# Kernel tuning notes

Hardware: AMD Instinct MI355X
Metric: run time of the kernel (lower is better)

Reference implementation:

```python
import jax, jax.numpy as jnp
import numpy as np

L, D, H, V, S, HID = 4, 1024, 16, 32000, 2048, 2816
HD = D // H  # 64
EPS = 1e-5


def setup_inputs() -> dict:
    key = jax.random.key(0)
    ks = jax.random.split(key, 10)
    s = 0.02  # init scale for numerical sanity; math is unaffected
    return {
        "tokens": jax.random.randint(ks[0], (1, S), 0, V),
        "emb": jax.random.normal(ks[1], (V, D), jnp.float32) * s,
        "wq": jax.random.normal(ks[2], (L, D, D), jnp.float32) * s,
        "wk": jax.random.normal(ks[3], (L, D, D), jnp.float32) * s,
        "wv": jax.random.normal(ks[4], (L, D, D), jnp.float32) * s,
        "wo": jax.random.normal(ks[5], (L, D, D), jnp.float32) * s,
        "w1": jax.random.normal(ks[6], (L, HID, D), jnp.float32) * s,
        "w2": jax.random.normal(ks[7], (L, D, HID), jnp.float32) * s,
        "w3": jax.random.normal(ks[8], (L, HID, D), jnp.float32) * s,
        "attn_norm_w": jnp.ones((L, D), jnp.float32),
        "ffn_norm_w": jnp.ones((L, D), jnp.float32),
        "final_norm_w": jnp.ones((D,), jnp.float32),
    }


def _rmsnorm(x, w):
    return x * jax.lax.rsqrt(jnp.mean(x * x, axis=-1, keepdims=True) + EPS) * w


def _rope(x, cos, sin):
    # x: [B,S,H,HD]; interleaved pairs (..., -1, 2) as in apply_rotary_emb
    xr, xi = x[..., 0::2], x[..., 1::2]
    outr = xr * cos - xi * sin
    outi = xr * sin + xi * cos
    return jnp.stack([outr, outi], axis=-1).reshape(x.shape)


def reference(tokens, emb, wq, wk, wv, wo, w1, w2, w3, attn_norm_w, ffn_norm_w, final_norm_w):
    # precompute_freqs_cis(head_dim, seq)
    inv_freq = 1.0 / (10000.0 ** (jnp.arange(0, HD, 2, dtype=jnp.float32) / HD))
    fr = jnp.outer(jnp.arange(S, dtype=jnp.float32), inv_freq)  # [S, HD/2]
    cos = jnp.cos(fr)[None, :, None, :]
    sin = jnp.sin(fr)[None, :, None, :]
    mask = jnp.triu(jnp.full((S, S), -jnp.inf, jnp.float32), k=1)
    scale = 1.0 / jnp.sqrt(jnp.float32(HD))

    h = emb[tokens]  # [B,S,D] embedding lookup (dropout p=0 -> identity)
    B = h.shape[0]

    def block(h, p):
        Wq, Wk, Wv, Wo, W1, W2, W3, anw, fnw = p
        x = _rmsnorm(h, anw)
        q = (x @ Wq.T).reshape(B, S, H, HD)
        k = (x @ Wk.T).reshape(B, S, H, HD)
        v = (x @ Wv.T).reshape(B, S, H, HD)
        q = _rope(q, cos, sin)
        k = _rope(k, cos, sin)
        q, k, v = (t.transpose(0, 2, 1, 3) for t in (q, k, v))  # [B,H,S,HD]
        scores = jnp.einsum("bhqd,bhkd->bhqk", q, k) * scale + mask
        attn = jax.nn.softmax(scores, axis=-1)
        o = jnp.einsum("bhqk,bhkd->bhqd", attn, v)
        o = o.transpose(0, 2, 1, 3).reshape(B, S, D)
        h = h + o @ Wo.T
        y = _rmsnorm(h, fnw)
        ff = (jax.nn.silu(y @ W1.T) * (y @ W3.T)) @ W2.T
        return h + ff, None

    h, _ = jax.lax.scan(block, h, (wq, wk, wv, wo, w1, w2, w3, attn_norm_w, ffn_norm_w))
    h = _rmsnorm(h, final_norm_w)
    logits = h[:, -1:, :] @ emb.T  # output weight tied to tok_embeddings; last position only
    return logits
```

## Files before the change

kernel.cpp:

```cpp
#include <hip/hip_runtime.h>

#define LNUM 4
#define DIM 1024
#define NH 16
#define VOCAB 32000
#define SEQ 2048
#define HIDD 2816

typedef _Float16 f16;
typedef _Float16 h8_t __attribute__((ext_vector_type(8)));
typedef _Float16 h4_t __attribute__((ext_vector_type(4)));
typedef float f4_t __attribute__((ext_vector_type(4)));

#define MFMA(a, b, c) __builtin_amdgcn_mfma_f32_16x16x32_f16(a, b, c, 0, 0, 0)

__device__ __forceinline__ void async16(void* lds, const void* g) {
  __builtin_amdgcn_global_load_lds(
      (const __attribute__((address_space(1))) void*)g,
      (__attribute__((address_space(3))) void*)lds, 16, 0, 0);
}

template <int N>
__device__ __forceinline__ float ror16(float x) {
  int r = __builtin_amdgcn_update_dpp(0, __builtin_bit_cast(int, x),
                                      0x120 | N, 0xF, 0xF, true);
  return __builtin_bit_cast(float, r);
}
__device__ __forceinline__ float rmax16(float v) {
  v = fmaxf(v, ror16<1>(v));
  v = fmaxf(v, ror16<2>(v));
  v = fmaxf(v, ror16<4>(v));
  v = fmaxf(v, ror16<8>(v));
  return v;
}
__device__ __forceinline__ float rsum16(float v) {
  v += ror16<1>(v);
  v += ror16<2>(v);
  v += ror16<4>(v);
  v += ror16<8>(v);
  return v;
}

__global__ __launch_bounds__(256) void cast_layer_k(
    const float* __restrict__ wq, const float* __restrict__ wk,
    const float* __restrict__ wv, const float* __restrict__ wo,
    const float* __restrict__ w1, const float* __restrict__ w3,
    const float* __restrict__ w2, f16* __restrict__ wqkv,
    f16* __restrict__ wod, f16* __restrict__ w13, f16* __restrict__ w2d) {
  const int DD4c = DIM * DIM / 4, HD4c = HIDD * DIM / 4;
  int i = blockIdx.x * 256 + threadIdx.x;
  const float* s;
  f16* d;
  int si, di;
  if (i < 3 * DD4c) {
    d = wqkv;
    di = i;
    if (i < DD4c) {
      s = wq; si = i;
    } else if (i < 2 * DD4c) {
      s = wk; si = i - DD4c;
    } else {
      s = wv; si = i - 2 * DD4c;
    }
  } else if (i < 4 * DD4c) {
    s = wo; si = i - 3 * DD4c; d = wod; di = si;
  } else if (i < 4 * DD4c + HD4c) {
    s = w1; si = i - 4 * DD4c; d = w13; di = si;
  } else if (i < 4 * DD4c + 2 * HD4c) {
    s = w3; si = i - 4 * DD4c - HD4c; d = w13; di = si + HD4c;
  } else {
    s = w2; si = i - 4 * DD4c - 2 * HD4c; d = w2d; di = si;
  }
  float4 v = ((const float4*)s)[si];
  ((h4_t*)d)[di] = (h4_t){(f16)v.x, (f16)v.y, (f16)v.z, (f16)v.w};
}

__global__ __launch_bounds__(256) void embed_k(const int* __restrict__ tok,
                                               const float* __restrict__ emb,
                                               float* __restrict__ h) {
  const int s = blockIdx.x, t = threadIdx.x;
  ((float4*)(h + (size_t)s * DIM))[t] =
      ((const float4*)(emb + (size_t)tok[s] * DIM))[t];
}

__global__ void rope_tab_k(float* __restrict__ tab) {
  int i = blockIdx.x * 256 + threadIdx.x;
  if (i >= SEQ * 32) return;
  int s = i >> 5, f = i & 31;
  float inv = powf(10000.f, -(float)f * (1.f / 32.f));
  float a = (float)s * inv;
  float sn, c;
  sincosf(a, &sn, &c);
  tab[i * 2] = c;
  tab[i * 2 + 1] = sn;
}

__global__ __launch_bounds__(256) void rope_k(f16* __restrict__ qkv,
                                              const float* __restrict__ tab) {
  int i = blockIdx.x * 256 + threadIdx.x;
  int f = i & 31, hh = (i >> 5) & 15, part = (i >> 9) & 1, s = i >> 10;
  size_t base = (size_t)s * 3072 + part * 1024 + hh * 64 + f * 2;
  float xr = (float)qkv[base], xi = (float)qkv[base + 1];
  float c = tab[(s * 32 + f) * 2], sn = tab[(s * 32 + f) * 2 + 1];
  qkv[base] = (f16)(xr * c - xi * sn);
  qkv[base + 1] = (f16)(xr * sn + xi * c);
}

__global__ __launch_bounds__(256) void rmsnorm_k(const float* __restrict__ h,
                                                 const float* __restrict__ w,
                                                 f16* __restrict__ out) {
  const int s = blockIdx.x, t = threadIdx.x;
  float4 v = ((const float4*)(h + (size_t)s * DIM))[t];
  float ss = v.x * v.x + v.y * v.y + v.z * v.z + v.w * v.w;
#pragma unroll
  for (int d = 1; d < 64; d <<= 1) ss += __shfl_xor(ss, d);
  __shared__ float red[4];
  if ((t & 63) == 0) red[t >> 6] = ss;
  __syncthreads();
  float tot = red[0] + red[1] + red[2] + red[3];
  float sc = rsqrtf(tot * (1.f / (float)DIM) + 1e-5f);
  float4 wv = ((const float4*)w)[t];
  ((h4_t*)(out + (size_t)s * DIM))[t] =
      (h4_t){(f16)(v.x * sc * wv.x), (f16)(v.y * sc * wv.y),
             (f16)(v.z * sc * wv.z), (f16)(v.w * sc * wv.w)};
}

__global__ __launch_bounds__(256) void final_norm_k(const float* __restrict__ h,
                                                    const float* __restrict__ w,
                                                    float* __restrict__ hn) {
  const int t = threadIdx.x;
  float4 v = ((const float4*)(h + (size_t)(SEQ - 1) * DIM))[t];
  float ss = v.x * v.x + v.y * v.y + v.z * v.z + v.w * v.w;
#pragma unroll
  for (int d = 1; d < 64; d <<= 1) ss += __shfl_xor(ss, d);
  __shared__ float red[4];
  if ((t & 63) == 0) red[t >> 6] = ss;
  __syncthreads();
  float tot = red[0] + red[1] + red[2] + red[3];
  float sc = rsqrtf(tot * (1.f / (float)DIM) + 1e-5f);
  float4 wv = ((const float4*)w)[t];
  ((float4*)hn)[t] = make_float4(v.x * sc * wv.x, v.y * sc * wv.y,
                                 v.z * sc * wv.z, v.w * sc * wv.w);
}

__global__ __launch_bounds__(256) void logits_k(const float* __restrict__ hn,
                                                const float* __restrict__ emb,
                                                float* __restrict__ out) {
  const int v = blockIdx.x * 4 + (threadIdx.x >> 6);
  const int lane = threadIdx.x & 63;
  const float4* er = (const float4*)(emb + (size_t)v * DIM);
  const float4* hr = (const float4*)hn;
  float s = 0.f;
#pragma unroll
  for (int i = 0; i < 4; i++) {
    float4 a = er[lane + i * 64];
    float4 b = hr[lane + i * 64];
    s += a.x * b.x + a.y * b.y + a.z * b.z + a.w * b.w;
  }
#pragma unroll
  for (int d = 1; d < 64; d <<= 1) s += __shfl_xor(s, d);
  if (lane == 0) out[v] = s;
}

__global__ __launch_bounds__(256) void silu_k(const f16* __restrict__ g13,
                                              f16* __restrict__ t) {
  int c = blockIdx.x * 256 + threadIdx.x;
  int s = blockIdx.y;
  float g = (float)g13[(size_t)s * (2 * HIDD) + c];
  float u = (float)g13[(size_t)s * (2 * HIDD) + HIDD + c];
  float r = g / (1.f + __expf(-g)) * u;
  t[(size_t)s * HIDD + c] = (f16)r;
}

__global__ __launch_bounds__(256) void transpose_v(const f16* __restrict__ qkv,
                                                   f16* __restrict__ vT) {
  __shared__ f16 tile[32][34];
  int bs = blockIdx.x * 32;
  int bc = blockIdx.y * 32;
  int tx = threadIdx.x & 31, ty = threadIdx.x >> 5;
#pragma unroll
  for (int i = ty; i < 32; i += 8)
    tile[i][tx] = qkv[(size_t)(bs + i) * 3072 + 2048 + bc + tx];
  __syncthreads();
#pragma unroll
  for (int i = ty; i < 32; i += 8)
    vT[(size_t)(bc + i) * SEQ + bs + tx] = tile[tx][i];
}

template <int EPI>
__global__ __launch_bounds__(256) void gemm_bt(const f16* __restrict__ A,
                                               const f16* __restrict__ B,
                                               void* __restrict__ Cout, int M,
                                               int N, int K) {
  __shared__ __align__(16) f16 As[128 * 32];
  __shared__ __align__(16) f16 Bs[128 * 32];
  const int t = threadIdx.x;
  const int lane = t & 63;
  const int wave = t >> 6;
  const int wr = wave >> 1, wc = wave & 1;
  const int bm = blockIdx.x, bn = blockIdx.y;
  const int lr = lane & 15, lk = lane >> 4;

  const int srow = t >> 2;
  const int scol = (t & 3) * 8;
  const f16* gA = A + (size_t)(bm * 128 + srow) * K + scol;
  const f16* gB = B + (size_t)(bn * 128 + srow) * K + scol;
  f16* lA = As + t * 8;
  f16* lB = Bs + t * 8;

  f4_t acc[4][4];
#pragma unroll
  for (int m = 0; m < 4; m++)
#pragma unroll
    for (int n = 0; n < 4; n++) acc[m][n] = {0.f, 0.f, 0.f, 0.f};

  for (int k0 = 0; k0 < K; k0 += 32) {
    __syncthreads();
    async16(lA, gA + k0);
    async16(lA + 64 * 32, gA + (size_t)64 * K + k0);
    async16(lB, gB + k0);
    async16(lB + 64 * 32, gB + (size_t)64 * K + k0);
    __syncthreads();
    h8_t af[4], bfr[4];
#pragma unroll
    for (int m = 0; m < 4; m++)
      af[m] = *(const h8_t*)(As + (wr * 64 + m * 16 + lr) * 32 + lk * 8);
#pragma unroll
    for (int n = 0; n < 4; n++)
      bfr[n] = *(const h8_t*)(Bs + (wc * 64 + n * 16 + lr) * 32 + lk * 8);
#pragma unroll
    for (int m = 0; m < 4; m++)
#pragma unroll
      for (int n = 0; n < 4; n++) acc[m][n] = MFMA(af[m], bfr[n], acc[m][n]);
  }

  const int orow = bm * 128 + wr * 64 + lk * 4;
  const int ocol = bn * 128 + wc * 64 + lr;
#pragma unroll
  for (int m = 0; m < 4; m++)
#pragma unroll
    for (int n = 0; n < 4; n++)
#pragma unroll
      for (int j = 0; j < 4; j++) {
        int r = orow + m * 16 + j;
        int c = ocol + n * 16;
        if (EPI == 0) {
          ((f16*)Cout)[(size_t)r * N + c] = (f16)acc[m][n][j];
        } else {
          float* pC = (float*)Cout + (size_t)r * N + c;
          *pC += acc[m][n][j];
        }
      }
}

__global__ __launch_bounds__(256) void gemm_skp(const f16* __restrict__ A,
                                                const f16* __restrict__ B,
                                                float* __restrict__ Cp, int N,
                                                int ld, int Ks) {
  __shared__ __align__(16) f16 As[128 * 32];
  __shared__ __align__(16) f16 Bs[128 * 32];
  const int t = threadIdx.x;
  const int lane = t & 63;
  const int wave = t >> 6;
  const int wr = wave >> 1, wc = wave & 1;
  const int bm = blockIdx.x, bn = blockIdx.y, bk = blockIdx.z;
  const int lr = lane & 15, lk = lane >> 4;

  const f16* Ao = A + (size_t)bk * Ks;
  const f16* Bo = B + (size_t)bk * Ks;
  float* Cout = Cp + (size_t)bk * gridDim.x * 128 * N;

  const int srow = t >> 2;
  const int scol = (t & 3) * 8;
  const f16* gA = Ao + (size_t)(bm * 128 + srow) * ld + scol;
  const f16* gB = Bo + (size_t)(bn * 128 + srow) * ld + scol;
  f16* lA = As + t * 8;
  f16* lB = Bs + t * 8;

  f4_t acc[4][4];
#pragma unroll
  for (int m = 0; m < 4; m++)
#pragma unroll
    for (int n = 0; n < 4; n++) acc[m][n] = {0.f, 0.f, 0.f, 0.f};

  for (int k0 = 0; k0 < Ks; k0 += 32) {
    __syncthreads();
    async16(lA, gA + k0);
    async16(lA + 64 * 32, gA + (size_t)64 * ld + k0);
    async16(lB, gB + k0);
    async16(lB + 64 * 32, gB + (size_t)64 * ld + k0);
    __syncthreads();
    h8_t af[4], bfr[4];
#pragma unroll
    for (int m = 0; m < 4; m++)
      af[m] = *(const h8_t*)(As + (wr * 64 + m * 16 + lr) * 32 + lk * 8);
#pragma unroll
    for (int n = 0; n < 4; n++)
      bfr[n] = *(const h8_t*)(Bs + (wc * 64 + n * 16 + lr) * 32 + lk * 8);
#pragma unroll
    for (int m = 0; m < 4; m++)
#pragma unroll
      for (int n = 0; n < 4; n++) acc[m][n] = MFMA(af[m], bfr[n], acc[m][n]);
  }

  const int orow = bm * 128 + wr * 64 + lk * 4;
  const int ocol = bn * 128 + wc * 64 + lr;
#pragma unroll
  for (int m = 0; m < 4; m++)
#pragma unroll
    for (int n = 0; n < 4; n++)
#pragma unroll
      for (int j = 0; j < 4; j++)
        Cout[(size_t)(orow + m * 16 + j) * N + ocol + n * 16] = acc[m][n][j];
}

__global__ __launch_bounds__(256) void sk_reduce_k(const float* __restrict__ p,
                                                   float* __restrict__ h,
                                                   int n4) {
  int i = blockIdx.x * 256 + threadIdx.x;
  if (i >= n4) return;
  float4 a = ((const float4*)p)[i];
  float4 b = ((const float4*)p)[i + n4];
  float4 c = ((float4*)h)[i];
  c.x += a.x + b.x;
  c.y += a.y + b.y;
  c.z += a.z + b.z;
  c.w += a.w + b.w;
  ((float4*)h)[i] = c;
}

__global__ __launch_bounds__(256) void attn_k(const f16* __restrict__ qkv,
                                              const f16* __restrict__ vT,
                                              f16* __restrict__ o) {
  const int hh = blockIdx.x;
  const int qb = blockIdx.y;
  const int tid = threadIdx.x;
  const int wave = tid >> 6;
  const int lane = tid & 63;
  const int lr = lane & 15, lk = lane >> 4;
  const int q0 = qb * 32;
  __shared__ __align__(16) char P[4][4096];
  __shared__ float MB[3][64][48];

  h8_t qf[2][2];
#pragma unroll
  for (int m = 0; m < 2; m++)
#pragma unroll
    for (int ks = 0; ks < 2; ks++)
      qf[m][ks] = *(const h8_t*)(qkv + (size_t)(q0 + m * 16 + lr) * 3072 +
                                 hh * 64 + ks * 32 + lk * 8);

  float mrow[2][4], lsum[2][4];
  f4_t oacc[2][4];
#pragma unroll
  for (int m = 0; m < 2; m++)
#pragma unroll
    for (int j = 0; j < 4; j++) {
      mrow[m][j] = -1e30f;
      lsum[m][j] = 0.f;
    }
#pragma unroll
  for (int m = 0; m < 2; m++)
#pragma unroll
    for (int n = 0; n < 4; n++) oacc[m][n] = {0.f, 0.f, 0.f, 0.f};

  const int ntiles = (qb >> 1) + 1;
  char* Pw = P[wave];
  for (int kt = wave; kt < ntiles; kt += 4) {
    f4_t sacc[2][4];
#pragma unroll
    for (int m = 0; m < 2; m++)
#pragma unroll
      for (int n = 0; n < 4; n++) sacc[m][n] = {0.f, 0.f, 0.f, 0.f};
#pragma unroll
    for (int ks = 0; ks < 2; ks++) {
      h8_t kf[4];
#pragma unroll
      for (int n = 0; n < 4; n++)
        kf[n] = *(const h8_t*)(qkv + (size_t)(kt * 64 + n * 16 + lr) * 3072 +
                               1024 + hh * 64 + ks * 32 + lk * 8);
#pragma unroll
      for (int m = 0; m < 2; m++)
#pragma unroll
        for (int n = 0; n < 4; n++)
          sacc[m][n] = MFMA(qf[m][ks], kf[n], sacc[m][n]);
    }
    const bool lastt = (kt == ntiles - 1);
    float pv[2][4][4];
#pragma unroll
    for (int m = 0; m < 2; m++)
#pragma unroll
      for (int n = 0; n < 4; n++)
#pragma unroll
        for (int j = 0; j < 4; j++) {
          float sv = sacc[m][n][j] * 0.125f;
          if (lastt && (kt * 64 + n * 16 + lr) > (q0 + m * 16 + lk * 4 + j))
            sv = -1e30f;
          pv[m][n][j] = sv;
        }
#pragma unroll
    for (int m = 0; m < 2; m++)
#pragma unroll
      for (int j = 0; j < 4; j++) {
        float mx = fmaxf(fmaxf(pv[m][0][j], pv[m][1][j]),
                         fmaxf(pv[m][2][j], pv[m][3][j]));
        mx = rmax16(mx);
        float mnew = fmaxf(mrow[m][j], mx);
        float corr = __expf(mrow[m][j] - mnew);
        mrow[m][j] = mnew;
        float rs = 0.f;
#pragma unroll
        for (int n = 0; n < 4; n++) {
          float pe = __expf(pv[m][n][j] - mnew);
          pv[m][n][j] = pe;
          rs += pe;
        }
        rs = rsum16(rs);
        lsum[m][j] = lsum[m][j] * corr + rs;
#pragma unroll
        for (int n = 0; n < 4; n++) oacc[m][n][j] *= corr;
      }
#pragma unroll
    for (int m = 0; m < 2; m++)
#pragma unroll
      for (int n = 0; n < 4; n++)
#pragma unroll
        for (int j = 0; j < 4; j++) {
          int r = m * 16 + lk * 4 + j, c = n * 16 + lr;
          int off = (r * 128 + c * 2) ^ ((r & 7) << 4);
          *(f16*)(Pw + off) = (f16)pv[m][n][j];
        }
#pragma unroll
    for (int ks = 0; ks < 2; ks++) {
      h8_t pf[2], vf[4];
#pragma unroll
      for (int m = 0; m < 2; m++) {
        int r = m * 16 + lr;
        int off = (r * 128 + ks * 64 + lk * 16) ^ ((r & 7) << 4);
        pf[m] = *(const h8_t*)(Pw + off);
      }
#pragma unroll
      for (int n = 0; n < 4; n++)
        vf[n] = *(const h8_t*)(vT + (size_t)(hh * 64 + n * 16 + lr) * SEQ +
                               kt * 64 + ks * 32 + lk * 8);
#pragma unroll
      for (int m = 0; m < 2; m++)
#pragma unroll
        for (int n = 0; n < 4; n++)
          oacc[m][n] = MFMA(pf[m], vf[n], oacc[m][n]);
    }
  }

  if (wave > 0) {
    float* d = &MB[wave - 1][lane][0];
#pragma unroll
    for (int m = 0; m < 2; m++)
#pragma unroll
      for (int j = 0; j < 4; j++) {
        d[m * 4 + j] = mrow[m][j];
        d[8 + m * 4 + j] = lsum[m][j];
      }
#pragma unroll
    for (int m = 0; m < 2; m++)
#pragma unroll
      for (int n = 0; n < 4; n++)
#pragma unroll
        for (int j = 0; j < 4; j++)
          d[16 + m * 16 + n * 4 + j] = oacc[m][n][j];
  }
  __syncthreads();
  if (wave == 0) {
#pragma unroll
    for (int m = 0; m < 2; m++)
#pragma unroll
      for (int j = 0; j < 4; j++) {
        float M = mrow[m][j];
#pragma unroll
        for (int w = 0; w < 3; w++) M = fmaxf(M, MB[w][lane][m * 4 + j]);
        float sc0 = __expf(mrow[m][j] - M);
        float L = lsum[m][j] * sc0;
        float scw[3];
#pragma unroll
        for (int w = 0; w < 3; w++) {
          scw[w] = __expf(MB[w][lane][m * 4 + j] - M);
          L += MB[w][lane][8 + m * 4 + j] * scw[w];
        }
        float invL = 1.f / L;
#pragma unroll
        for (int n = 0; n < 4; n++) {
          float val = oacc[m][n][j] * sc0;
#pragma unroll
          for (int w = 0; w < 3; w++)
            val += MB[w][lane][16 + m * 16 + n * 4 + j] * scw[w];
          o[(size_t)(q0 + m * 16 + lk * 4 + j) * DIM + hh * 64 + n * 16 + lr] =
              (f16)(val * invL);
        }
      }
  }
}

extern "C" void kernel_launch(void* const* d_in, const int* in_sizes, int n_in,
                              void* d_out, int out_size, void* d_ws,
                              size_t ws_size, hipStream_t stream) {
  (void)in_sizes; (void)n_in; (void)out_size; (void)ws_size;
  const int* tokens = (const int*)d_in[0];
  const float* emb = (const float*)d_in[1];
  const float* wq = (const float*)d_in[2];
  const float* wk = (const float*)d_in[3];
  const float* wv = (const float*)d_in[4];
  const float* wo = (const float*)d_in[5];
  const float* w1 = (const float*)d_in[6];
  const float* w2 = (const float*)d_in[7];
  const float* w3 = (const float*)d_in[8];
  const float* anw = (const float*)d_in[9];
  const float* fnw = (const float*)d_in[10];
  const float* finw = (const float*)d_in[11];
  float* out = (float*)d_out;

  char* p = (char*)d_ws;
  auto alloc = [&](size_t bytes) {
    char* r = p;
    p += (bytes + 255) & ~(size_t)255;
    return r;
  };
  f16* wqkv_l = (f16*)alloc((size_t)3 * DIM * DIM * 2);
  f16* wo_l = (f16*)alloc((size_t)DIM * DIM * 2);
  f16* w13_l = (f16*)alloc((size_t)2 * HIDD * DIM * 2);
  f16* w2_l = (f16*)alloc((size_t)DIM * HIDD * 2);
  float* hbuf = (float*)alloc((size_t)SEQ * DIM * 4);
  f16* x_h = (f16*)alloc((size_t)SEQ * DIM * 2);
  f16* qkv_h = (f16*)alloc((size_t)SEQ * 3 * DIM * 2);
  f16* vT_h = (f16*)alloc((size_t)DIM * SEQ * 2);
  f16* o_h = (f16*)alloc((size_t)SEQ * DIM * 2);
  f16* g13_h = (f16*)alloc((size_t)SEQ * 2 * HIDD * 2);
  f16* t_h = (f16*)alloc((size_t)SEQ * HIDD * 2);
  float* skbuf = (float*)alloc((size_t)2 * SEQ * DIM * 4);
  float* tab = (float*)alloc((size_t)SEQ * 32 * 2 * 4);
  float* hn = (float*)alloc(4096);

  embed_k<<<SEQ, 256, 0, stream>>>(tokens, emb, hbuf);
  rope_tab_k<<<(SEQ * 32 + 255) / 256, 256, 0, stream>>>(tab);

  const int CAST_BLOCKS = (4 * (DIM * DIM / 4) + 3 * (HIDD * DIM / 4)) / 256;
  const int N4 = SEQ * DIM / 4;
  for (int l = 0; l < LNUM; l++) {
    const size_t offDD = (size_t)l * DIM * DIM;
    const size_t offHD = (size_t)l * HIDD * DIM;
    cast_layer_k<<<CAST_BLOCKS, 256, 0, stream>>>(
        wq + offDD, wk + offDD, wv + offDD, wo + offDD, w1 + offHD,
        w3 + offHD, w2 + offHD, wqkv_l, wo_l, w13_l, w2_l);

    rmsnorm_k<<<SEQ, 256, 0, stream>>>(hbuf, anw + (size_t)l * DIM, x_h);
    {
      dim3 g(SEQ / 128, (3 * DIM) / 128);
      gemm_bt<0><<<g, 256, 0, stream>>>(x_h, wqkv_l, qkv_h, SEQ, 3 * DIM, DIM);
    }
    rope_k<<<(SEQ * 2 * NH * 32) / 256, 256, 0, stream>>>(qkv_h, tab);
    {
      dim3 g(SEQ / 32, DIM / 32);
      transpose_v<<<g, 256, 0, stream>>>(qkv_h, vT_h);
    }
    {
      dim3 g(NH, SEQ / 32);
      attn_k<<<g, 256, 0, stream>>>(qkv_h, vT_h, o_h);
    }
    {
      dim3 g(SEQ / 128, DIM / 128, 2);
      gemm_skp<<<g, 256, 0, stream>>>(o_h, wo_l, skbuf, DIM, DIM, DIM / 2);
      sk_reduce_k<<<(N4 + 255) / 256, 256, 0, stream>>>(skbuf, hbuf, N4);
    }
    rmsnorm_k<<<SEQ, 256, 0, stream>>>(hbuf, fnw + (size_t)l * DIM, x_h);
    {
      dim3 g(SEQ / 128, (2 * HIDD) / 128);
      gemm_bt<0><<<g, 256, 0, stream>>>(x_h, w13_l, g13_h, SEQ, 2 * HIDD, DIM);
    }
    {
      dim3 g(HIDD / 256, SEQ);
      silu_k<<<g, 256, 0, stream>>>(g13_h, t_h);
    }
    {
      dim3 g(SEQ / 128, DIM / 128, 2);
      gemm_skp<<<g, 256, 0, stream>>>(t_h, w2_l, skbuf, DIM, HIDD, HIDD / 2);
      sk_reduce_k<<<(N4 + 255) / 256, 256, 0, stream>>>(skbuf, hbuf, N4);
    }
  }
  final_norm_k<<<1, 256, 0, stream>>>(hbuf, finw, hn);
  logits_k<<<VOCAB / 4, 256, 0, stream>>>(hn, emb, out);
}
```

Measured before the change: 896.1 us.

## Fuse RoPE, SiLU-gate and split-K reduction into GEMM epilogues

Applies RoPE in the QKV GEMM epilogue via DPP lane swaps, and fuses the W1/W3 GEMMs with the SiLU gating into one kernel that holds two accumulator sets. The split-K GEMMs now atomically add straight into the residual buffer, so the partial-sum buffer and reduce kernel are gone. Attention merge scratch for O is stored in fp16 to cut LDS use. This removes several kernel launches and intermediate HBM round trips, at the cost of doubled accumulator registers in the W13 kernel, nondeterministic fp32 atomics, and slightly lower precision in the attention merge.

```diff
diff --git a/kernel.cpp b/kernel.cpp
--- a/kernel.cpp
+++ b/kernel.cpp
@@ -39,6 +39,11 @@
   v += ror16<4>(v);
   v += ror16<8>(v);
   return v;
+}
+__device__ __forceinline__ float qswap(float x) {
+  int r = __builtin_amdgcn_update_dpp(0, __builtin_bit_cast(int, x), 0xB1,
+                                      0xF, 0xF, true);
+  return __builtin_bit_cast(float, r);
 }
 
 __global__ __launch_bounds__(256) void cast_layer_k(
@@ -95,17 +100,6 @@
   tab[i * 2 + 1] = sn;
 }
 
-__global__ __launch_bounds__(256) void rope_k(f16* __restrict__ qkv,
-                                              const float* __restrict__ tab) {
-  int i = blockIdx.x * 256 + threadIdx.x;
-  int f = i & 31, hh = (i >> 5) & 15, part = (i >> 9) & 1, s = i >> 10;
-  size_t base = (size_t)s * 3072 + part * 1024 + hh * 64 + f * 2;
-  float xr = (float)qkv[base], xi = (float)qkv[base + 1];
-  float c = tab[(s * 32 + f) * 2], sn = tab[(s * 32 + f) * 2 + 1];
-  qkv[base] = (f16)(xr * c - xi * sn);
-  qkv[base + 1] = (f16)(xr * sn + xi * c);
-}
-
 __global__ __launch_bounds__(256) void rmsnorm_k(const float* __restrict__ h,
                                                  const float* __restrict__ w,
                                                  f16* __restrict__ out) {
@@ -162,16 +156,6 @@
   if (lane == 0) out[v] = s;
 }
 
-__global__ __launch_bounds__(256) void silu_k(const f16* __restrict__ g13,
-                                              f16* __restrict__ t) {
-  int c = blockIdx.x * 256 + threadIdx.x;
-  int s = blockIdx.y;
-  float g = (float)g13[(size_t)s * (2 * HIDD) + c];
-  float u = (float)g13[(size_t)s * (2 * HIDD) + HIDD + c];
-  float r = g / (1.f + __expf(-g)) * u;
-  t[(size_t)s * HIDD + c] = (f16)r;
-}
-
 __global__ __launch_bounds__(256) void transpose_v(const f16* __restrict__ qkv,
                                                    f16* __restrict__ vT) {
   __shared__ f16 tile[32][34];
@@ -187,11 +171,11 @@
     vT[(size_t)(bc + i) * SEQ + bs + tx] = tile[tx][i];
 }
 
-template <int EPI>
-__global__ __launch_bounds__(256) void gemm_bt(const f16* __restrict__ A,
-                                               const f16* __restrict__ B,
-                                               void* __restrict__ Cout, int M,
-                                               int N, int K) {
+__global__ __launch_bounds__(256) void gemm_qkv(const f16* __restrict__ A,
+                                                const f16* __restrict__ B,
+                                                f16* __restrict__ C,
+                                                const float* __restrict__ tab) {
+  const int N = 3 * DIM, K = DIM;
   __shared__ __align__(16) f16 As[128 * 32];
   __shared__ __align__(16) f16 Bs[128 * 32];
   const int t = threadIdx.x;
@@ -236,27 +220,102 @@
 
   const int orow = bm * 128 + wr * 64 + lk * 4;
   const int ocol = bn * 128 + wc * 64 + lr;
+  const float ssign = (lr & 1) ? 1.f : -1.f;
 #pragma unroll
   for (int m = 0; m < 4; m++)
 #pragma unroll
-    for (int n = 0; n < 4; n++)
+    for (int n = 0; n < 4; n++) {
+      const int c = ocol + n * 16;
+      const bool qk = c < 2048;
+      const int f = (n * 16 + lr) >> 1;
 #pragma unroll
       for (int j = 0; j < 4; j++) {
         int r = orow + m * 16 + j;
-        int c = ocol + n * 16;
-        if (EPI == 0) {
-          ((f16*)Cout)[(size_t)r * N + c] = (f16)acc[m][n][j];
-        } else {
-          float* pC = (float*)Cout + (size_t)r * N + c;
-          *pC += acc[m][n][j];
+        float sv = acc[m][n][j];
+        float pa = qswap(sv);
+        if (qk) {
+          float2 cs = ((const float2*)tab)[r * 32 + f];
+          sv = sv * cs.x + pa * cs.y * ssign;
         }
+        C[(size_t)r * N + c] = (f16)sv;
+      }
+    }
+}
+
+__global__ __launch_bounds__(256) void gemm_w13(const f16* __restrict__ A,
+                                                const f16* __restrict__ B13,
+                                                f16* __restrict__ T) {
+  const int K = DIM;
+  __shared__ __align__(16) f16 As[128 * 32];
+  __shared__ __align__(16) f16 B1s[128 * 32];
+  __shared__ __align__(16) f16 B3s[128 * 32];
+  const int t = threadIdx.x;
+  const int lane = t & 63;
+  const int wave = t >> 6;
+  const int wr = wave >> 1, wc = wave & 1;
+  const int bm = blockIdx.x, bn = blockIdx.y;
+  const int lr = lane & 15, lk = lane >> 4;
+
+  const int srow = t >> 2;
+  const int scol = (t & 3) * 8;
+  const f16* gA = A + (size_t)(bm * 128 + srow) * K + scol;
+  const f16* gB1 = B13 + (size_t)(bn * 128 + srow) * K + scol;
+  const f16* gB3 = B13 + (size_t)(HIDD + bn * 128 + srow) * K + scol;
+  f16* lA = As + t * 8;
+  f16* lB1 = B1s + t * 8;
+  f16* lB3 = B3s + t * 8;
+
+  f4_t acc1[4][4], acc3[4][4];
+#pragma unroll
+  for (int m = 0; m < 4; m++)
+#pragma unroll
+    for (int n = 0; n < 4; n++) {
+      acc1[m][n] = {0.f, 0.f, 0.f, 0.f};
+      acc3[m][n] = {0.f, 0.f, 0.f, 0.f};
+    }
+
+  for (int k0 = 0; k0 < K; k0 += 32) {
+    __syncthreads();
+    async16(lA, gA + k0);
+    async16(lA + 64 * 32, gA + (size_t)64 * K + k0);
+    async16(lB1, gB1 + k0);
+    async16(lB1 + 64 * 32, gB1 + (size_t)64 * K + k0);
+    async16(lB3, gB3 + k0);
+    async16(lB3 + 64 * 32, gB3 + (size_t)64 * K + k0);
+    __syncthreads();
+    h8_t af[4];
+#pragma unroll
+    for (int m = 0; m < 4; m++)
+      af[m] = *(const h8_t*)(As + (wr * 64 + m * 16 + lr) * 32 + lk * 8);
+#pragma unroll
+    for (int n = 0; n < 4; n++) {
+      h8_t b1 = *(const h8_t*)(B1s + (wc * 64 + n * 16 + lr) * 32 + lk * 8);
+#pragma unroll
+      for (int m = 0; m < 4; m++) acc1[m][n] = MFMA(af[m], b1, acc1[m][n]);
+      h8_t b3 = *(const h8_t*)(B3s + (wc * 64 + n * 16 + lr) * 32 + lk * 8);
+#pragma unroll
+      for (int m = 0; m < 4; m++) acc3[m][n] = MFMA(af[m], b3, acc3[m][n]);
+    }
+  }
+
+  const int orow = bm * 128 + wr * 64 + lk * 4;
+  const int ocol = bn * 128 + wc * 64 + lr;
+#pragma unroll
+  for (int m = 0; m < 4; m++)
+#pragma unroll
+    for (int n = 0; n < 4; n++)
+#pragma unroll
+      for (int j = 0; j < 4; j++) {
+        float g = acc1[m][n][j], u = acc3[m][n][j];
+        float r = g / (1.f + __expf(-g)) * u;
+        T[(size_t)(orow + m * 16 + j) * HIDD + ocol + n * 16] = (f16)r;
       }
 }
 
 __global__ __launch_bounds__(256) void gemm_skp(const f16* __restrict__ A,
                                                 const f16* __restrict__ B,
-                                                float* __restrict__ Cp, int N,
-                                                int ld, int Ks) {
+                                                float* __restrict__ H, int ld,
+                                                int Ks) {
   __shared__ __align__(16) f16 As[128 * 32];
   __shared__ __align__(16) f16 Bs[128 * 32];
   const int t = threadIdx.x;
@@ -268,7 +327,6 @@
 
   const f16* Ao = A + (size_t)bk * Ks;
   const f16* Bo = B + (size_t)bk * Ks;
-  float* Cout = Cp + (size_t)bk * gridDim.x * 128 * N;
 
   const int srow = t >> 2;
   const int scol = (t & 3) * 8;
@@ -311,22 +369,8 @@
     for (int n = 0; n < 4; n++)
 #pragma unroll
       for (int j = 0; j < 4; j++)
-        Cout[(size_t)(orow + m * 16 + j) * N + ocol + n * 16] = acc[m][n][j];
-}
-
-__global__ __launch_bounds__(256) void sk_reduce_k(const float* __restrict__ p,
-                                                   float* __restrict__ h,
-                                                   int n4) {
-  int i = blockIdx.x * 256 + threadIdx.x;
-  if (i >= n4) return;
-  float4 a = ((const float4*)p)[i];
-  float4 b = ((const float4*)p)[i + n4];
-  float4 c = ((float4*)h)[i];
-  c.x += a.x + b.x;
-  c.y += a.y + b.y;
-  c.z += a.z + b.z;
-  c.w += a.w + b.w;
-  ((float4*)h)[i] = c;
+        atomicAdd(H + (size_t)(orow + m * 16 + j) * DIM + ocol + n * 16,
+                  acc[m][n][j]);
 }
 
 __global__ __launch_bounds__(256) void attn_k(const f16* __restrict__ qkv,
@@ -340,7 +384,8 @@
   const int lr = lane & 15, lk = lane >> 4;
   const int q0 = qb * 32;
   __shared__ __align__(16) char P[4][4096];
-  __shared__ float MB[3][64][48];
+  __shared__ float MBml[3][64][16];
+  __shared__ f16 MBo[3][64][32];
 
   h8_t qf[2][2];
 #pragma unroll
@@ -452,13 +497,14 @@
   }
 
   if (wave > 0) {
-    float* d = &MB[wave - 1][lane][0];
+    float* dml = &MBml[wave - 1][lane][0];
+    f16* doo = &MBo[wave - 1][lane][0];
 #pragma unroll
     for (int m = 0; m < 2; m++)
 #pragma unroll
       for (int j = 0; j < 4; j++) {
-        d[m * 4 + j] = mrow[m][j];
-        d[8 + m * 4 + j] = lsum[m][j];
+        dml[m * 4 + j] = mrow[m][j];
+        dml[8 + m * 4 + j] = lsum[m][j];
       }
 #pragma unroll
     for (int m = 0; m < 2; m++)
@@ -466,7 +512,7 @@
       for (int n = 0; n < 4; n++)
 #pragma unroll
         for (int j = 0; j < 4; j++)
-          d[16 + m * 16 + n * 4 + j] = oacc[m][n][j];
+          doo[m * 16 + n * 4 + j] = (f16)oacc[m][n][j];
   }
   __syncthreads();
   if (wave == 0) {
@@ -476,14 +522,14 @@
       for (int j = 0; j < 4; j++) {
         float M = mrow[m][j];
 #pragma unroll
-        for (int w = 0; w < 3; w++) M = fmaxf(M, MB[w][lane][m * 4 + j]);
+        for (int w = 0; w < 3; w++) M = fmaxf(M, MBml[w][lane][m * 4 + j]);
         float sc0 = __expf(mrow[m][j] - M);
         float L = lsum[m][j] * sc0;
         float scw[3];
 #pragma unroll
         for (int w = 0; w < 3; w++) {
-          scw[w] = __expf(MB[w][lane][m * 4 + j] - M);
-          L += MB[w][lane][8 + m * 4 + j] * scw[w];
+          scw[w] = __expf(MBml[w][lane][m * 4 + j] - M);
+          L += MBml[w][lane][8 + m * 4 + j] * scw[w];
         }
         float invL = 1.f / L;
 #pragma unroll
@@ -491,7 +537,7 @@
           float val = oacc[m][n][j] * sc0;
 #pragma unroll
           for (int w = 0; w < 3; w++)
-            val += MB[w][lane][16 + m * 16 + n * 4 + j] * scw[w];
+            val += (float)MBo[w][lane][m * 16 + n * 4 + j] * scw[w];
           o[(size_t)(q0 + m * 16 + lk * 4 + j) * DIM + hh * 64 + n * 16 + lr] =
               (f16)(val * invL);
         }
@@ -532,9 +578,7 @@
   f16* qkv_h = (f16*)alloc((size_t)SEQ * 3 * DIM * 2);
   f16* vT_h = (f16*)alloc((size_t)DIM * SEQ * 2);
   f16* o_h = (f16*)alloc((size_t)SEQ * DIM * 2);
-  f16* g13_h = (f16*)alloc((size_t)SEQ * 2 * HIDD * 2);
   f16* t_h = (f16*)alloc((size_t)SEQ * HIDD * 2);
-  float* skbuf = (float*)alloc((size_t)2 * SEQ * DIM * 4);
   float* tab = (float*)alloc((size_t)SEQ * 32 * 2 * 4);
   float* hn = (float*)alloc(4096);
 
@@ -542,7 +586,6 @@
   rope_tab_k<<<(SEQ * 32 + 255) / 256, 256, 0, stream>>>(tab);
 
   const int CAST_BLOCKS = (4 * (DIM * DIM / 4) + 3 * (HIDD * DIM / 4)) / 256;
-  const int N4 = SEQ * DIM / 4;
   for (int l = 0; l < LNUM; l++) {
     const size_t offDD = (size_t)l * DIM * DIM;
     const size_t offHD = (size_t)l * HIDD * DIM;
@@ -553,9 +596,8 @@
     rmsnorm_k<<<SEQ, 256, 0, stream>>>(hbuf, anw + (size_t)l * DIM, x_h);
     {
       dim3 g(SEQ / 128, (3 * DIM) / 128);
-      gemm_bt<0><<<g, 256, 0, stream>>>(x_h, wqkv_l, qkv_h, SEQ, 3 * DIM, DIM);
-    }
-    rope_k<<<(SEQ * 2 * NH * 32) / 256, 256, 0, stream>>>(qkv_h, tab);
+      gemm_qkv<<<g, 256, 0, stream>>>(x_h, wqkv_l, qkv_h, tab);
+    }
     {
       dim3 g(SEQ / 32, DIM / 32);
       transpose_v<<<g, 256, 0, stream>>>(qkv_h, vT_h);
@@ -566,22 +608,16 @@
     }
     {
       dim3 g(SEQ / 128, DIM / 128, 2);
-      gemm_skp<<<g, 256, 0, stream>>>(o_h, wo_l, skbuf, DIM, DIM, DIM / 2);
-      sk_reduce_k<<<(N4 + 255) / 256, 256, 0, stream>>>(skbuf, hbuf, N4);
+      gemm_skp<<<g, 256, 0, stream>>>(o_h, wo_l, hbuf, DIM, DIM / 2);
     }
     rmsnorm_k<<<SEQ, 256, 0, stream>>>(hbuf, fnw + (size_t)l * DIM, x_h);
     {
-      dim3 g(SEQ / 128, (2 * HIDD) / 128);
-      gemm_bt<0><<<g, 256, 0, stream>>>(x_h, w13_l, g13_h, SEQ, 2 * HIDD, DIM);
-    }
-    {
-      dim3 g(HIDD / 256, SEQ);
-      silu_k<<<g, 256, 0, stream>>>(g13_h, t_h);
+      dim3 g(SEQ / 128, HIDD / 128);
+      gemm_w13<<<g, 256, 0, stream>>>(x_h, w13_l, t_h);
     }
     {
       dim3 g(SEQ / 128, DIM / 128, 2);
-      gemm_skp<<<g, 256, 0, stream>>>(t_h, w2_l, skbuf, DIM, HIDD, HIDD / 2);
-      sk_reduce_k<<<(N4 + 255) / 256, 256, 0, stream>>>(skbuf, hbuf, N4);
+      gemm_skp<<<g, 256, 0, stream>>>(t_h, w2_l, hbuf, HIDD, HIDD / 2);
     }
   }
   final_norm_k<<<1, 256, 0, stream>>>(hbuf, finw, hn);
```

Result: slower. 1.030 ms (+14.9%).
